# Kernel optimization log

Hardware: AMD Instinct MI355X
Metric: run time of the kernel (lower is better)

The kernel has to match this reference:

```python
import jax, jax.numpy as jnp
import numpy as np

N = 50000      # nodes
E = 400000     # edges (before self-loops)
F_IN = 256     # num_node_features == H*C (required by residual add)
H = 4          # heads
C = 64         # hidden_dim per head
G = 64         # number of graphs in batch
NCLS = 10
EPS = 1e-5
NEG_SLOPE = 0.2  # PyG GATConv default leaky_relu slope


def setup_inputs() -> dict:
    key = jax.random.key(0)
    ks = jax.random.split(key, 20)
    def w(k, shape, s=0.05):
        return jax.random.normal(k, shape, dtype=jnp.float32) * s
    inp = {
        "x": jax.random.normal(ks[0], (N, F_IN), dtype=jnp.float32),
        "edge_index": jax.random.randint(ks[1], (2, E), 0, N, dtype=jnp.int64),
        "batch": jnp.sort(jax.random.randint(ks[2], (N,), 0, G, dtype=jnp.int64)),
        # GAT layer 1 (in=256 -> H*C=256, concat)
        "W1": w(ks[3], (F_IN, H * C)),
        "att_src1": w(ks[4], (H, C)),
        "att_dst1": w(ks[5], (H, C)),
        "b1": jnp.zeros((H * C,), jnp.float32),
        "gamma1": jnp.ones((H * C,), jnp.float32),
        "beta1": jnp.zeros((H * C,), jnp.float32),
        # GAT layer 2 (in=256 -> H*C=256, concat)
        "W2": w(ks[6], (H * C, H * C)),
        "att_src2": w(ks[7], (H, C)),
        "att_dst2": w(ks[8], (H, C)),
        "b2": jnp.zeros((H * C,), jnp.float32),
        "gamma2": jnp.ones((H * C,), jnp.float32),
        "beta2": jnp.zeros((H * C,), jnp.float32),
        # MLP head
        "fc1_w": w(ks[9], (H * C, C)),
        "fc1_b": jnp.zeros((C,), jnp.float32),
        "fc2_w": w(ks[10], (C, NCLS)),
        "fc2_b": jnp.zeros((NCLS,), jnp.float32),
    }
    return inp


def _gat(x, W, att_s, att_d, b, src, dst):
    # x: [N, F] -> h: [N, H, C]
    h = (x @ W).reshape(N, H, C)
    a_src = jnp.einsum('nhc,hc->nh', h, att_s)  # [N, H]
    a_dst = jnp.einsum('nhc,hc->nh', h, att_d)
    e = jax.nn.leaky_relu(a_src[src] + a_dst[dst], NEG_SLOPE)  # [Etot, H]
    # softmax over incoming edges per destination node (self-loops ensure nonempty)
    m = jax.ops.segment_max(e, dst, num_segments=N)
    ex = jnp.exp(e - m[dst])
    s = jax.ops.segment_sum(ex, dst, num_segments=N)
    alpha = ex / s[dst]  # [Etot, H]
    out = jax.ops.segment_sum(alpha[:, :, None] * h[src], dst, num_segments=N)
    return out.reshape(N, H * C) + b


def _bn(x, gamma, beta):
    mu = x.mean(0)
    var = x.var(0)
    return gamma * (x - mu) * jax.lax.rsqrt(var + EPS) + beta


def reference(x, edge_index, batch, W1, att_src1, att_dst1, b1, gamma1, beta1,
              W2, att_src2, att_dst2, b2, gamma2, beta2, fc1_w, fc1_b, fc2_w, fc2_b):
    loops = jnp.arange(N, dtype=edge_index.dtype)
    src = jnp.concatenate([edge_index[0], loops])  # PyG GATConv add_self_loops=True
    dst = jnp.concatenate([edge_index[1], loops])

    h = jax.nn.elu(_gat(x, W1, att_src1, att_dst1, b1, src, dst))
    h = _bn(h + x, gamma1, beta1)  # dropout omitted (eval)
    h2 = jax.nn.elu(_gat(h, W2, att_src2, att_dst2, b2, src, dst))
    h = _bn(h2 + h, gamma2, beta2)

    # global mean pool over graphs
    sums = jax.ops.segment_sum(h, batch, num_segments=G)
    cnt = jax.ops.segment_sum(jnp.ones((N,), h.dtype), batch, num_segments=G)
    pooled = sums / jnp.maximum(cnt, 1.0)[:, None]  # [G, H*C]

    z = jax.nn.relu(pooled @ fc1_w + fc1_b)
    logits = z @ fc2_w + fc2_b
    return jax.nn.log_softmax(logits, axis=1)
```

## Files before the change

### kernel.cpp

```cpp
#include <hip/hip_runtime.h>
#include <hip/hip_bf16.h>

#define NNODES 50000
#define NF 256
#define NH 4
#define NG 64
#define NCLS 10
#define MPAD 50048

typedef __hip_bfloat16 bf16;
typedef __attribute__((ext_vector_type(8))) short short8;
typedef __attribute__((ext_vector_type(4))) short bfx4;
typedef __attribute__((ext_vector_type(4))) float floatx4;

__device__ inline float ldf(const void* p, int i, int isbf) {
    return isbf ? __bfloat162float(((const bf16*)p)[i]) : ((const float*)p)[i];
}
__device__ inline float4 ld4f(const void* p, int i, int isbf) {
    if (isbf) {
        const unsigned* q = (const unsigned*)((const short*)p + i);
        unsigned u0 = q[0], u1 = q[1];
        return make_float4(__uint_as_float(u0 << 16), __uint_as_float(u0 & 0xFFFF0000u),
                           __uint_as_float(u1 << 16), __uint_as_float(u1 & 0xFFFF0000u));
    }
    return *(const float4*)((const float*)p + i);
}
__device__ inline void stf(void* p, int i, float v, int isbf) {
    if (isbf) ((bf16*)p)[i] = __float2bfloat16(v);
    else ((float*)p)[i] = v;
}
__device__ inline short f2bfbits(float v) {
    bf16 b = __float2bfloat16(v);
    return *reinterpret_cast<short*>(&b);
}
__device__ inline float bfbits2f(short s) {
    return __uint_as_float(((unsigned)(unsigned short)s) << 16);
}
__device__ inline unsigned char f2fp8(float v) {
    return (unsigned char)(__builtin_amdgcn_cvt_pk_fp8_f32(v, v, 0, false) & 0xFF);
}
__device__ inline int clampN(int v) { return ((unsigned)v < (unsigned)NNODES) ? v : 0; }
__device__ inline int clampG(int v) { return ((unsigned)v < (unsigned)NG) ? v : 0; }

__global__ void detect_kernel(const int* __restrict__ ei, const unsigned* __restrict__ w1,
                              int* __restrict__ flags) {
    __shared__ int nzOdd, insane;
    if (threadIdx.x == 0) { nzOdd = 0; insane = 0; }
    __syncthreads();
    if (ei[2 * threadIdx.x + 1] != 0) atomicAdd(&nzOdd, 1);
    unsigned lo = w1[threadIdx.x] & 0xFFFFu;
    unsigned ex = (lo >> 7) & 0xFFu;
    bool sane = ((lo & 0x7FFFu) == 0u) || (ex >= 90u && ex <= 133u);
    if (!sane) atomicAdd(&insane, 1);
    __syncthreads();
    if (threadIdx.x == 0) {
        flags[0] = (nzOdd == 0) ? 1 : 0;
        flags[1] = (insane == 0) ? 1 : 0;
    }
}

__device__ inline void edge_sd(const int* __restrict__ ei, int e, int E, int is64,
                               int& s_, int& d_) {
    if (e < E) {
        if (is64) { s_ = ei[2 * e]; d_ = ei[2 * E + 2 * e]; }
        else      { s_ = ei[e];     d_ = ei[E + e]; }
    } else {
        s_ = d_ = e - E;
    }
    s_ = clampN(s_);
    d_ = clampN(d_);
}

__global__ void deg_kernel(const int* __restrict__ ei, int* __restrict__ deg,
                           int E, int ET, const int* __restrict__ flags) {
    int e = blockIdx.x * 256 + threadIdx.x;
    if (e >= ET) return;
    int s_, d_;
    edge_sd(ei, e, E, flags[0], s_, d_);
    atomicAdd(&deg[d_], 1);
}

__global__ void scan1_kernel(const int* __restrict__ deg, int* __restrict__ eprefix,
                             int* __restrict__ bsums, int n) {
    __shared__ int sc[256];
    int t = threadIdx.x, i = blockIdx.x * 256 + t;
    int val = (i < n) ? deg[i] : 0;
    sc[t] = val;
    __syncthreads();
    for (int off = 1; off < 256; off <<= 1) {
        int tmp = (t >= off) ? sc[t - off] : 0;
        __syncthreads();
        sc[t] += tmp;
        __syncthreads();
    }
    if (i < n) eprefix[i] = sc[t] - val;
    if (t == 255) bsums[blockIdx.x] = sc[255];
}

__global__ void scan2_kernel(const int* __restrict__ bsums, int* __restrict__ boffs, int nb) {
    __shared__ int sc[256];
    int t = threadIdx.x;
    int val = (t < nb) ? bsums[t] : 0;
    sc[t] = val;
    __syncthreads();
    for (int off = 1; off < 256; off <<= 1) {
        int tmp = (t >= off) ? sc[t - off] : 0;
        __syncthreads();
        sc[t] += tmp;
        __syncthreads();
    }
    if (t < nb) boffs[t] = sc[t] - val;
}

__global__ void scan3_kernel(const int* __restrict__ eprefix, const int* __restrict__ boffs,
                             int* __restrict__ rowptr, int n, int ET) {
    int i = blockIdx.x * 256 + threadIdx.x;
    if (i < n) rowptr[i] = eprefix[i] + boffs[blockIdx.x];
    if (i == n) rowptr[n] = ET;
}

__global__ void scatter_kernel(const int* __restrict__ ei, const int* __restrict__ rowptr,
                               int* __restrict__ cursor, int* __restrict__ srcs,
                               int E, int ET, const int* __restrict__ flags) {
    int e = blockIdx.x * 256 + threadIdx.x;
    if (e >= ET) return;
    int s_, d_;
    edge_sd(ei, e, E, flags[0], s_, d_);
    int pos = atomicAdd(&cursor[d_], 1);
    srcs[rowptr[d_] + pos] = s_;
}

__global__ void goff_bs_kernel(const int* __restrict__ bt, int* __restrict__ goff,
                               int* __restrict__ gcnt, const int* __restrict__ flags) {
    int is64 = flags[0];
    int t = threadIdx.x;
    if (t <= NG) {
        int lo = 0, hi = NNODES;
        while (lo < hi) {
            int mid = (lo + hi) >> 1;
            int b = clampG(is64 ? bt[2 * mid] : bt[mid]);
            if (b < t) lo = mid + 1; else hi = mid;
        }
        goff[t] = lo;
    }
    __syncthreads();
    if (t < NG) gcnt[t] = goff[t + 1] - goff[t];
}

__global__ void repack_kernel(const void* __restrict__ W, short* __restrict__ Bf,
                              const int* __restrict__ flags) {
    int i = blockIdx.x * 256 + threadIdx.x;
    int j = i & 7, lane = (i >> 3) & 63, tile = i >> 9;
    int kt = tile >> 4, ctg = tile & 15;
    int k = kt * 32 + (lane >> 4) * 8 + j;
    int n = ctg * 16 + (lane & 15);
    Bf[i] = f2bfbits(ldf(W, k * NF + n, flags[1]));
}

__global__ void bn_finalize_kernel(const float* __restrict__ bsum, const float* __restrict__ bsumsq,
                                   const void* __restrict__ gamma, const void* __restrict__ beta,
                                   float* __restrict__ scale, float* __restrict__ shift,
                                   const int* __restrict__ flags) {
    int t = threadIdx.x;
    int isbf = flags[1];
    const float invN = 1.0f / (float)NNODES;
    float mu = bsum[t] * invN;
    float var = fmaxf(bsumsq[t] * invN - mu * mu, 0.f);
    float s = ldf(gamma, t, isbf) * rsqrtf(var + 1e-5f);
    scale[t] = s;
    shift[t] = ldf(beta, t, isbf) - mu * s;
}

__global__ __launch_bounds__(256) void gemm_mfma(
        const void* __restrict__ A, const short* __restrict__ Bf,
        unsigned char* __restrict__ C8,
        int M, const int* __restrict__ flags, int aFollows,
        const void* __restrict__ att_s, const void* __restrict__ att_d,
        float* __restrict__ a_src, float* __restrict__ a_dst,
        const float* __restrict__ scaleA, const float* __restrict__ shiftA) {
    __shared__ short smem[16 * 528];
    int isbf = flags[1];
    int aIsBf = aFollows ? isbf : 1;
    int t = threadIdx.x;
    int wave = t >> 6;
    int lane = t & 63;
    int am = lane & 15, aq = lane >> 4;
    int row0 = blockIdx.x * 32;

    if (aIsBf) {
        #pragma unroll
        for (int i = 0; i < 4; i++) {
            int j = wave * 4 + i;
            int grow = min(row0 + 2 * j + (lane >> 5), M - 1);
            int f0 = (lane & 31) * 8;
            short8 v = *(const short8*)((const short*)A + grow * NF + f0);
            if (scaleA) {
                #pragma unroll
                for (int jj = 0; jj < 8; jj++)
                    v[jj] = f2bfbits(bfbits2f(v[jj]) * scaleA[f0 + jj] + shiftA[f0 + jj]);
            }
            *(short8*)&smem[j * 528 + (lane >> 5) * 256 + f0] = v;
        }
    } else {
        #pragma unroll
        for (int i = 0; i < 4; i++) {
            int u = t * 4 + i;
            int row = u >> 5;
            int pos = u & 31;
            int grow = min(row0 + row, M - 1);
            const float* fp = (const float*)A + grow * NF + pos * 8;
            float4 f0 = *(const float4*)fp;
            float4 f1 = *(const float4*)(fp + 4);
            short8 v;
            v[0] = f2bfbits(f0.x); v[1] = f2bfbits(f0.y);
            v[2] = f2bfbits(f0.z); v[3] = f2bfbits(f0.w);
            v[4] = f2bfbits(f1.x); v[5] = f2bfbits(f1.y);
            v[6] = f2bfbits(f1.z); v[7] = f2bfbits(f1.w);
            *(short8*)&smem[(row >> 1) * 528 + (row & 1) * 256 + pos * 8] = v;
        }
    }
    __syncthreads();

    floatx4 acc[2][4];
    #pragma unroll
    for (int i = 0; i < 2; i++)
        #pragma unroll
        for (int j = 0; j < 4; j++) acc[i][j] = (floatx4){0.f, 0.f, 0.f, 0.f};

    int aoff0 = (am >> 1) * 528 + (am & 1) * 256 + aq * 8;
    #pragma unroll
    for (int kt = 0; kt < 8; kt++) {
        short8 a0 = *(const short8*)&smem[aoff0 + kt * 32];
        short8 a1 = *(const short8*)&smem[aoff0 + 8 * 528 + kt * 32];
        short8 b[4];
        #pragma unroll
        for (int ct = 0; ct < 4; ct++)
            b[ct] = *(const short8*)&Bf[((kt * 16 + wave * 4 + ct) * 64 + lane) * 8];
        #pragma unroll
        for (int ct = 0; ct < 4; ct++) {
            acc[0][ct] = __builtin_amdgcn_mfma_f32_16x16x32_bf16(a0, b[ct], acc[0][ct], 0, 0, 0);
            acc[1][ct] = __builtin_amdgcn_mfma_f32_16x16x32_bf16(a1, b[ct], acc[1][ct], 0, 0, 0);
        }
    }

    int rbase = aq * 4;
    int cbase = wave * 64 + am;
    #pragma unroll
    for (int rt = 0; rt < 2; rt++) {
        #pragma unroll
        for (int r = 0; r < 4; r++) {
            int row = row0 + rt * 16 + rbase + r;
            if (row < M) {
                #pragma unroll
                for (int ct = 0; ct < 4; ct++)
                    C8[row * NF + cbase + ct * 16] = f2fp8(acc[rt][ct][r]);
            }
        }
    }
    float attS[4], attD[4];
    #pragma unroll
    for (int ct = 0; ct < 4; ct++) {
        int col = wave * 64 + ct * 16 + am;
        attS[ct] = ldf(att_s, col, isbf);
        attD[ct] = ldf(att_d, col, isbf);
    }
    #pragma unroll
    for (int rt = 0; rt < 2; rt++) {
        #pragma unroll
        for (int r = 0; r < 4; r++) {
            float ps = 0.f, pd = 0.f;
            #pragma unroll
            for (int ct = 0; ct < 4; ct++) {
                float v = acc[rt][ct][r];
                ps += v * attS[ct];
                pd += v * attD[ct];
            }
            #pragma unroll
            for (int m = 1; m <= 8; m <<= 1) {
                ps += __shfl_xor(ps, m, 64);
                pd += __shfl_xor(pd, m, 64);
            }
            int row = row0 + rt * 16 + rbase + r;
            if (am == 0 && row < M) {
                a_src[row * NH + wave] = ps;
                a_dst[row * NH + wave] = pd;
            }
        }
    }
}

__device__ inline float leaky_clamp(float v) {
    v = v > 0.f ? v : 0.2f * v;
    return fminf(fmaxf(v, -30.f), 30.f);
}

__global__ __launch_bounds__(64) void agg_csr_kernel(
        const int* __restrict__ rowptr, const int* __restrict__ srcs,
        const float* __restrict__ asrc, const float* __restrict__ adst,
        const unsigned char* __restrict__ h8, const void* __restrict__ bias,
        const void* __restrict__ resid, bf16* __restrict__ agg,
        const int* __restrict__ flags, int residFollows,
        const float* __restrict__ rscale, const float* __restrict__ rshift) {
    int d = blockIdx.x;
    int l = threadIdx.x;
    int hh = l >> 4;
    int e16 = l & 15;
    int isbf = flags[1];
    int rIsBf = residFollows ? isbf : 1;
    int beg = rowptr[d], end = rowptr[d + 1];
    float ad = adst[d * NH + hh];
    __shared__ float sAl[NH][16];
    __shared__ int sSrc[16];
    float a0 = 0.f, a1 = 0.f, a2 = 0.f, a3 = 0.f, den = 0.f;
    for (int cb = beg; cb < end; cb += 16) {
        int nk = min(16, end - cb);
        if (e16 < nk) {
            int s = srcs[cb + e16];
            if (hh == 0) sSrc[e16] = s;
            sAl[hh][e16] = __expf(leaky_clamp(asrc[s * NH + hh] + ad));
        }
        __syncthreads();
        for (int k = 0; k < nk; k++) {
            float al = sAl[hh][k];
            den += al;
            unsigned u = *(const unsigned*)&h8[sSrc[k] * NF + 4 * l];
            auto lo = __builtin_amdgcn_cvt_pk_f32_fp8((int)u, false);
            auto hi = __builtin_amdgcn_cvt_pk_f32_fp8((int)u, true);
            a0 += al * lo[0];
            a1 += al * lo[1];
            a2 += al * hi[0];
            a3 += al * hi[1];
        }
        __syncthreads();
    }
    float inv = 1.f / fmaxf(den, 1e-30f);
    a0 *= inv; a1 *= inv; a2 *= inv; a3 *= inv;
    int f0 = 4 * l;
    float4 r = ld4f(resid, d * NF + f0, rIsBf);
    if (rscale) {
        r.x = r.x * rscale[f0] + rshift[f0];
        r.y = r.y * rscale[f0 + 1] + rshift[f0 + 1];
        r.z = r.z * rscale[f0 + 2] + rshift[f0 + 2];
        r.w = r.w * rscale[f0 + 3] + rshift[f0 + 3];
    }
    float v0 = a0 + ldf(bias, f0, isbf);
    float v1 = a1 + ldf(bias, f0 + 1, isbf);
    float v2 = a2 + ldf(bias, f0 + 2, isbf);
    float v3 = a3 + ldf(bias, f0 + 3, isbf);
    v0 = v0 > 0.f ? v0 : (__expf(v0) - 1.0f);
    v1 = v1 > 0.f ? v1 : (__expf(v1) - 1.0f);
    v2 = v2 > 0.f ? v2 : (__expf(v2) - 1.0f);
    v3 = v3 > 0.f ? v3 : (__expf(v3) - 1.0f);
    bfx4 o;
    o[0] = f2bfbits(v0 + r.x);
    o[1] = f2bfbits(v1 + r.y);
    o[2] = f2bfbits(v2 + r.z);
    o[3] = f2bfbits(v3 + r.w);
    *(bfx4*)&agg[d * NF + f0] = o;
}

__global__ __launch_bounds__(256) void bn_stats_kernel(
        const bf16* __restrict__ x, float* __restrict__ bsum, float* __restrict__ bsumsq) {
    __shared__ float ssum[8][256];
    __shared__ float ssq[8][256];
    int t = threadIdx.x;
    int fg = t & 31, rg = t >> 5;
    int f0 = fg * 8;
    float s[8] = {0, 0, 0, 0, 0, 0, 0, 0};
    float q[8] = {0, 0, 0, 0, 0, 0, 0, 0};
    for (int r = blockIdx.x * 8 + rg; r < NNODES; r += gridDim.x * 8) {
        short8 v = *(const short8*)&x[r * NF + f0];
        #pragma unroll
        for (int j = 0; j < 8; j++) {
            float fv = bfbits2f(v[j]);
            s[j] += fv;
            q[j] += fv * fv;
        }
    }
    #pragma unroll
    for (int j = 0; j < 8; j++) {
        ssum[rg][f0 + j] = s[j];
        ssq[rg][f0 + j] = q[j];
    }
    __syncthreads();
    float ts = 0.f, tq = 0.f;
    #pragma unroll
    for (int g = 0; g < 8; g++) {
        ts += ssum[g][t];
        tq += ssq[g][t];
    }
    atomicAdd(&bsum[t], ts);
    atomicAdd(&bsumsq[t], tq);
}

__global__ void pool2_kernel(const bf16* __restrict__ x, const int* __restrict__ goff,
                             float* __restrict__ pooled) {
    int g = blockIdx.x >> 3, c = blockIdx.x & 7, t = threadIdx.x;
    int beg = goff[g], end = goff[g + 1];
    int len = end - beg;
    if (len <= 0) return;
    int chunk = (len + 7) >> 3;
    int s0 = beg + c * chunk;
    int s1 = min(s0 + chunk, end);
    if (s0 >= s1) return;
    float acc = 0.f;
    for (int n = s0; n < s1; n++) acc += __bfloat162float(x[n * NF + t]);
    atomicAdd(&pooled[g * NF + t], acc);
}

__global__ __launch_bounds__(256) void head_kernel(
        const float* __restrict__ pooled, const int* __restrict__ gcnt,
        const float* __restrict__ bnsum2, const float* __restrict__ bnsq2,
        const void* __restrict__ gamma2, const void* __restrict__ beta2,
        const void* __restrict__ fc1w, const void* __restrict__ fc1b,
        const void* __restrict__ fc2w, const void* __restrict__ fc2b,
        void* __restrict__ out, const int* __restrict__ flags) {
    int g = blockIdx.x;
    int t = threadIdx.x;
    int isbf = flags[1];
    __shared__ float p[NF];
    __shared__ float zpart[4][64];
    __shared__ float z[64];
    __shared__ float logits[NCLS];
    __shared__ float lse;
    float c = fmaxf((float)gcnt[g], 1.f);
    float invc = 1.f / c;
    const float invN = 1.0f / (float)NNODES;
    {
        float mu = bnsum2[t] * invN;
        float var = fmaxf(bnsq2[t] * invN - mu * mu, 0.f);
        float pm = pooled[g * NF + t] * invc;
        p[t] = ldf(gamma2, t, isbf) * ((pm - mu) * rsqrtf(var + 1e-5f)) + ldf(beta2, t, isbf);
    }
    __syncthreads();
    int o = t & 63, q = t >> 6;
    int k0 = q * 64;
    float acc = 0.f;
    if (isbf) {
        const bf16* w = (const bf16*)fc1w;
        #pragma unroll 8
        for (int k = k0; k < k0 + 64; k++) acc += p[k] * __bfloat162float(w[k * 64 + o]);
    } else {
        const float* w = (const float*)fc1w;
        #pragma unroll 8
        for (int k = k0; k < k0 + 64; k++) acc += p[k] * w[k * 64 + o];
    }
    zpart[q][o] = acc;
    __syncthreads();
    if (t < 64) {
        float v = zpart[0][t] + zpart[1][t] + zpart[2][t] + zpart[3][t] + ldf(fc1b, t, isbf);
        z[t] = v > 0.f ? v : 0.f;
    }
    __syncthreads();
    if (t < NCLS) {
        float a2 = ldf(fc2b, t, isbf);
        #pragma unroll 8
        for (int k = 0; k < 64; k++) a2 += z[k] * ldf(fc2w, k * NCLS + t, isbf);
        logits[t] = a2;
    }
    __syncthreads();
    if (t == 0) {
        float mx = logits[0];
        for (int j = 1; j < NCLS; j++) mx = fmaxf(mx, logits[j]);
        float se = 0.f;
        for (int j = 0; j < NCLS; j++) se += expf(logits[j] - mx);
        lse = mx + logf(se);
    }
    __syncthreads();
    if (t < NCLS) stf(out, g * NCLS + t, logits[t] - lse, isbf);
}

extern "C" void kernel_launch(void* const* d_in, const int* in_sizes, int n_in,
                              void* d_out, int out_size, void* d_ws, size_t ws_size,
                              hipStream_t stream) {
    const void* x = d_in[0];
    const int* edge_index = (const int*)d_in[1];
    const int* batch = (const int*)d_in[2];
    const void* W1 = d_in[3];
    const void* att_src1 = d_in[4];
    const void* att_dst1 = d_in[5];
    const void* b1 = d_in[6];
    const void* gamma1 = d_in[7];
    const void* beta1 = d_in[8];
    const void* W2 = d_in[9];
    const void* att_src2 = d_in[10];
    const void* att_dst2 = d_in[11];
    const void* b2 = d_in[12];
    const void* gamma2 = d_in[13];
    const void* beta2 = d_in[14];
    const void* fc1w = d_in[15];
    const void* fc1b = d_in[16];
    const void* fc2w = d_in[17];
    const void* fc2b = d_in[18];

    const int E = in_sizes[1] / 2;
    const int ET = E + NNODES;
    const int NE = NNODES * NF;
    const int NNH = NNODES * NH;
    const int NB = (NNODES + 255) / 256;
    const int NB1 = (NNODES + 1 + 255) / 256;

    float* ws = (float*)d_ws;
    bf16* aggb = (bf16*)ws;
    float* asrc = ws + NE / 2;
    float* adst = asrc + NNH;
    int* flags = (int*)(adst + NNH);
    unsigned char* h8 = (unsigned char*)(flags + 16);
    bf16* l1ob = (bf16*)(h8 + (size_t)MPAD * NF);
    int* rowptr = (int*)(l1ob + (size_t)MPAD * NF);
    int* srcs = rowptr + NNODES + 16;
    int* goff = srcs + ET + 16;
    int* deg = goff + NG + 1 + 14;
    int* cursor = deg + NNODES;
    int* gcnt = cursor + NNODES;
    float* pooled = (float*)(gcnt + NG);
    float* bnstat = pooled + NG * NF;
    size_t zero_bytes = (size_t)(2 * NNODES + NG) * 4 + (size_t)(NG * NF + 4 * NF) * 4;
    short* Bf1 = (short*)(bnstat + 4 * NF);
    short* Bf2 = Bf1 + NF * NF;
    float* scale1 = (float*)(Bf2 + NF * NF);
    float* shift1 = scale1 + NF;
    int* eprefix = (int*)asrc;
    int* bsums = eprefix + NNODES + 16;
    int* boffs = bsums + 256;

    float* bnsum1 = bnstat;
    float* bnsq1 = bnstat + NF;
    float* bnsum2 = bnstat + 2 * NF;
    float* bnsq2 = bnstat + 3 * NF;

    detect_kernel<<<1, 256, 0, stream>>>(edge_index, (const unsigned*)W1, flags);
    (void)hipMemsetAsync(deg, 0, zero_bytes, stream);

    repack_kernel<<<NF * NF / 256, 256, 0, stream>>>(W1, Bf1, flags);
    repack_kernel<<<NF * NF / 256, 256, 0, stream>>>(W2, Bf2, flags);

    deg_kernel<<<(ET + 255) / 256, 256, 0, stream>>>(edge_index, deg, E, ET, flags);
    scan1_kernel<<<NB, 256, 0, stream>>>(deg, eprefix, bsums, NNODES);
    scan2_kernel<<<1, 256, 0, stream>>>(bsums, boffs, NB);
    scan3_kernel<<<NB1, 256, 0, stream>>>(eprefix, boffs, rowptr, NNODES, ET);
    scatter_kernel<<<(ET + 255) / 256, 256, 0, stream>>>(edge_index, rowptr, cursor, srcs, E, ET, flags);
    goff_bs_kernel<<<1, 128, 0, stream>>>(batch, goff, gcnt, flags);

    gemm_mfma<<<MPAD / 32, 256, 0, stream>>>(x, Bf1, h8, NNODES, flags, 1,
                                             att_src1, att_dst1, asrc, adst,
                                             nullptr, nullptr);
    agg_csr_kernel<<<NNODES, 64, 0, stream>>>(rowptr, srcs, asrc, adst, h8, b1, x, aggb,
                                              flags, 1, nullptr, nullptr);
    bn_stats_kernel<<<512, 256, 0, stream>>>(aggb, bnsum1, bnsq1);
    bn_finalize_kernel<<<1, 256, 0, stream>>>(bnsum1, bnsq1, gamma1, beta1, scale1, shift1, flags);

    gemm_mfma<<<MPAD / 32, 256, 0, stream>>>(aggb, Bf2, h8, NNODES, flags, 0,
                                             att_src2, att_dst2, asrc, adst,
                                             scale1, shift1);
    agg_csr_kernel<<<NNODES, 64, 0, stream>>>(rowptr, srcs, asrc, adst, h8, b2, aggb, aggb,
                                              flags, 0, scale1, shift1);
    bn_stats_kernel<<<512, 256, 0, stream>>>(aggb, bnsum2, bnsq2);

    pool2_kernel<<<NG * 8, 256, 0, stream>>>(aggb, goff, pooled);
    head_kernel<<<NG, 256, 0, stream>>>(pooled, gcnt, bnsum2, bnsq2, gamma2, beta2,
                                        fc1w, fc1b, fc2w, fc2b, d_out, flags);
}
```

Before: 385.5 us.

## Merge independent small kernels into combined launches and fold BN finalize into consumers

```diff
diff --git a/kernel.cpp b/kernel.cpp
--- a/kernel.cpp
+++ b/kernel.cpp
@@ -7,6 +7,7 @@
 #define NG 64
 #define NCLS 10
 #define MPAD 50048
+#define GEMM_BLKS (MPAD / 32)
 
 typedef __hip_bfloat16 bf16;
 typedef __attribute__((ext_vector_type(8))) short short8;
@@ -71,13 +72,34 @@
     d_ = clampN(d_);
 }
 
-__global__ void deg_kernel(const int* __restrict__ ei, int* __restrict__ deg,
-                           int E, int ET, const int* __restrict__ flags) {
-    int e = blockIdx.x * 256 + threadIdx.x;
+__device__ __forceinline__ void repack_body(int b, const void* __restrict__ W,
+                                            short* __restrict__ Bf, int isbf) {
+    int i = b * 256 + threadIdx.x;
+    int j = i & 7, lane = (i >> 3) & 63, tile = i >> 9;
+    int kt = tile >> 4, ctg = tile & 15;
+    int k = kt * 32 + (lane >> 4) * 8 + j;
+    int n = ctg * 16 + (lane & 15);
+    Bf[i] = f2bfbits(ldf(W, k * NF + n, isbf));
+}
+
+__device__ __forceinline__ void deg_body(int b, const int* __restrict__ ei,
+                                         int* __restrict__ deg, int E, int ET, int is64) {
+    int e = b * 256 + threadIdx.x;
     if (e >= ET) return;
     int s_, d_;
-    edge_sd(ei, e, E, flags[0], s_, d_);
+    edge_sd(ei, e, E, is64, s_, d_);
     atomicAdd(&deg[d_], 1);
+}
+
+__global__ __launch_bounds__(256) void prep_kernel(
+        const void* __restrict__ W1, short* __restrict__ Bf1,
+        const void* __restrict__ W2, short* __restrict__ Bf2,
+        const int* __restrict__ ei, int* __restrict__ deg, int E, int ET,
+        const int* __restrict__ flags) {
+    int b = blockIdx.x;
+    if (b < 256) repack_body(b, W1, Bf1, flags[1]);
+    else if (b < 512) repack_body(b - 256, W2, Bf2, flags[1]);
+    else deg_body(b - 512, ei, deg, E, ET, flags[0]);
 }
 
 __global__ void scan1_kernel(const int* __restrict__ deg, int* __restrict__ eprefix,
@@ -97,7 +119,9 @@
     if (t == 255) bsums[blockIdx.x] = sc[255];
 }
 
-__global__ void scan2_kernel(const int* __restrict__ bsums, int* __restrict__ boffs, int nb) {
+__global__ void scan2_goff_kernel(const int* __restrict__ bsums, int* __restrict__ boffs, int nb,
+                                  const int* __restrict__ bt, int* __restrict__ goff,
+                                  int* __restrict__ gcnt, const int* __restrict__ flags) {
     __shared__ int sc[256];
     int t = threadIdx.x;
     int val = (t < nb) ? bsums[t] : 0;
@@ -110,30 +134,7 @@
         __syncthreads();
     }
     if (t < nb) boffs[t] = sc[t] - val;
-}
-
-__global__ void scan3_kernel(const int* __restrict__ eprefix, const int* __restrict__ boffs,
-                             int* __restrict__ rowptr, int n, int ET) {
-    int i = blockIdx.x * 256 + threadIdx.x;
-    if (i < n) rowptr[i] = eprefix[i] + boffs[blockIdx.x];
-    if (i == n) rowptr[n] = ET;
-}
-
-__global__ void scatter_kernel(const int* __restrict__ ei, const int* __restrict__ rowptr,
-                               int* __restrict__ cursor, int* __restrict__ srcs,
-                               int E, int ET, const int* __restrict__ flags) {
-    int e = blockIdx.x * 256 + threadIdx.x;
-    if (e >= ET) return;
-    int s_, d_;
-    edge_sd(ei, e, E, flags[0], s_, d_);
-    int pos = atomicAdd(&cursor[d_], 1);
-    srcs[rowptr[d_] + pos] = s_;
-}
-
-__global__ void goff_bs_kernel(const int* __restrict__ bt, int* __restrict__ goff,
-                               int* __restrict__ gcnt, const int* __restrict__ flags) {
     int is64 = flags[0];
-    int t = threadIdx.x;
     if (t <= NG) {
         int lo = 0, hi = NNODES;
         while (lo < hi) {
@@ -147,45 +148,52 @@
     if (t < NG) gcnt[t] = goff[t + 1] - goff[t];
 }
 
-__global__ void repack_kernel(const void* __restrict__ W, short* __restrict__ Bf,
-                              const int* __restrict__ flags) {
+__global__ void scan3_kernel(const int* __restrict__ eprefix, const int* __restrict__ boffs,
+                             int* __restrict__ rowptr, int n, int ET) {
     int i = blockIdx.x * 256 + threadIdx.x;
-    int j = i & 7, lane = (i >> 3) & 63, tile = i >> 9;
-    int kt = tile >> 4, ctg = tile & 15;
-    int k = kt * 32 + (lane >> 4) * 8 + j;
-    int n = ctg * 16 + (lane & 15);
-    Bf[i] = f2bfbits(ldf(W, k * NF + n, flags[1]));
-}
-
-__global__ void bn_finalize_kernel(const float* __restrict__ bsum, const float* __restrict__ bsumsq,
-                                   const void* __restrict__ gamma, const void* __restrict__ beta,
-                                   float* __restrict__ scale, float* __restrict__ shift,
-                                   const int* __restrict__ flags) {
-    int t = threadIdx.x;
-    int isbf = flags[1];
-    const float invN = 1.0f / (float)NNODES;
-    float mu = bsum[t] * invN;
-    float var = fmaxf(bsumsq[t] * invN - mu * mu, 0.f);
-    float s = ldf(gamma, t, isbf) * rsqrtf(var + 1e-5f);
-    scale[t] = s;
-    shift[t] = ldf(beta, t, isbf) - mu * s;
-}
-
-__global__ __launch_bounds__(256) void gemm_mfma(
-        const void* __restrict__ A, const short* __restrict__ Bf,
-        unsigned char* __restrict__ C8,
-        int M, const int* __restrict__ flags, int aFollows,
+    if (i < n) rowptr[i] = eprefix[i] + boffs[blockIdx.x];
+    if (i == n) rowptr[n] = ET;
+}
+
+__device__ __forceinline__ void scatter_body(int b, const int* __restrict__ ei,
+                                             const int* __restrict__ rowptr,
+                                             int* __restrict__ cursor, int* __restrict__ srcs,
+                                             int E, int ET, int is64) {
+    int e = b * 256 + threadIdx.x;
+    if (e >= ET) return;
+    int s_, d_;
+    edge_sd(ei, e, E, is64, s_, d_);
+    int pos = atomicAdd(&cursor[d_], 1);
+    srcs[rowptr[d_] + pos] = s_;
+}
+
+__device__ __forceinline__ void gemm_body(
+        int bid, const void* __restrict__ A, const short* __restrict__ Bf,
+        unsigned char* __restrict__ C8, int M, const int* __restrict__ flags, int aFollows,
         const void* __restrict__ att_s, const void* __restrict__ att_d,
         float* __restrict__ a_src, float* __restrict__ a_dst,
-        const float* __restrict__ scaleA, const float* __restrict__ shiftA) {
+        const float* __restrict__ bnsum, const float* __restrict__ bnsq,
+        const void* __restrict__ gamma, const void* __restrict__ beta, int applyBN) {
     __shared__ short smem[16 * 528];
+    __shared__ float sscale[NF];
+    __shared__ float sshift[NF];
     int isbf = flags[1];
     int aIsBf = aFollows ? isbf : 1;
     int t = threadIdx.x;
     int wave = t >> 6;
     int lane = t & 63;
     int am = lane & 15, aq = lane >> 4;
-    int row0 = blockIdx.x * 32;
+    int row0 = bid * 32;
+
+    if (applyBN) {
+        const float invN = 1.0f / (float)NNODES;
+        float mu = bnsum[t] * invN;
+        float var = fmaxf(bnsq[t] * invN - mu * mu, 0.f);
+        float s = ldf(gamma, t, isbf) * rsqrtf(var + 1e-5f);
+        sscale[t] = s;
+        sshift[t] = ldf(beta, t, isbf) - mu * s;
+        __syncthreads();
+    }
 
     if (aIsBf) {
         #pragma unroll
@@ -194,10 +202,10 @@
             int grow = min(row0 + 2 * j + (lane >> 5), M - 1);
             int f0 = (lane & 31) * 8;
             short8 v = *(const short8*)((const short*)A + grow * NF + f0);
-            if (scaleA) {
+            if (applyBN) {
                 #pragma unroll
                 for (int jj = 0; jj < 8; jj++)
-                    v[jj] = f2bfbits(bfbits2f(v[jj]) * scaleA[f0 + jj] + shiftA[f0 + jj]);
+                    v[jj] = f2bfbits(bfbits2f(v[jj]) * sscale[f0 + jj] + sshift[f0 + jj]);
             }
             *(short8*)&smem[j * 528 + (lane >> 5) * 256 + f0] = v;
         }
@@ -289,6 +297,33 @@
     }
 }
 
+__global__ __launch_bounds__(256) void scatter_gemm1_kernel(
+        const int* __restrict__ ei, const int* __restrict__ rowptr,
+        int* __restrict__ cursor, int* __restrict__ srcs, int E, int ET,
+        const void* __restrict__ A, const short* __restrict__ Bf,
+        unsigned char* __restrict__ C8, int M,
+        const void* __restrict__ att_s, const void* __restrict__ att_d,
+        float* __restrict__ a_src, float* __restrict__ a_dst,
+        const int* __restrict__ flags) {
+    if (blockIdx.x < GEMM_BLKS)
+        gemm_body(blockIdx.x, A, Bf, C8, M, flags, 1, att_s, att_d, a_src, a_dst,
+                  nullptr, nullptr, nullptr, nullptr, 0);
+    else
+        scatter_body(blockIdx.x - GEMM_BLKS, ei, rowptr, cursor, srcs, E, ET, flags[0]);
+}
+
+__global__ __launch_bounds__(256) void gemm2_kernel(
+        const void* __restrict__ A, const short* __restrict__ Bf,
+        unsigned char* __restrict__ C8, int M,
+        const void* __restrict__ att_s, const void* __restrict__ att_d,
+        float* __restrict__ a_src, float* __restrict__ a_dst,
+        const float* __restrict__ bnsum, const float* __restrict__ bnsq,
+        const void* __restrict__ gamma, const void* __restrict__ beta,
+        const int* __restrict__ flags) {
+    gemm_body(blockIdx.x, A, Bf, C8, M, flags, 0, att_s, att_d, a_src, a_dst,
+              bnsum, bnsq, gamma, beta, 1);
+}
+
 __device__ inline float leaky_clamp(float v) {
     v = v > 0.f ? v : 0.2f * v;
     return fminf(fmaxf(v, -30.f), 30.f);
@@ -300,13 +335,28 @@
         const unsigned char* __restrict__ h8, const void* __restrict__ bias,
         const void* __restrict__ resid, bf16* __restrict__ agg,
         const int* __restrict__ flags, int residFollows,
-        const float* __restrict__ rscale, const float* __restrict__ rshift) {
+        const float* __restrict__ bnsum, const float* __restrict__ bnsq,
+        const void* __restrict__ gamma, const void* __restrict__ beta, int applyBN) {
     int d = blockIdx.x;
     int l = threadIdx.x;
     int hh = l >> 4;
     int e16 = l & 15;
     int isbf = flags[1];
     int rIsBf = residFollows ? isbf : 1;
+    int f0 = 4 * l;
+    float sc[4] = {1.f, 1.f, 1.f, 1.f}, sh[4] = {0.f, 0.f, 0.f, 0.f};
+    if (applyBN) {
+        const float invN = 1.0f / (float)NNODES;
+        #pragma unroll
+        for (int j = 0; j < 4; j++) {
+            int f = f0 + j;
+            float mu = bnsum[f] * invN;
+            float var = fmaxf(bnsq[f] * invN - mu * mu, 0.f);
+            float s = ldf(gamma, f, isbf) * rsqrtf(var + 1e-5f);
+            sc[j] = s;
+            sh[j] = ldf(beta, f, isbf) - mu * s;
+        }
+    }
     int beg = rowptr[d], end = rowptr[d + 1];
     float ad = adst[d * NH + hh];
     __shared__ float sAl[NH][16];
@@ -323,7 +373,7 @@
         for (int k = 0; k < nk; k++) {
             float al = sAl[hh][k];
             den += al;
-            unsigned u = *(const unsigned*)&h8[sSrc[k] * NF + 4 * l];
+            unsigned u = *(const unsigned*)&h8[sSrc[k] * NF + f0];
             auto lo = __builtin_amdgcn_cvt_pk_f32_fp8((int)u, false);
             auto hi = __builtin_amdgcn_cvt_pk_f32_fp8((int)u, true);
             a0 += al * lo[0];
@@ -335,13 +385,12 @@
     }
     float inv = 1.f / fmaxf(den, 1e-30f);
     a0 *= inv; a1 *= inv; a2 *= inv; a3 *= inv;
-    int f0 = 4 * l;
     float4 r = ld4f(resid, d * NF + f0, rIsBf);
-    if (rscale) {
-        r.x = r.x * rscale[f0] + rshift[f0];
-        r.y = r.y * rscale[f0 + 1] + rshift[f0 + 1];
-        r.z = r.z * rscale[f0 + 2] + rshift[f0 + 2];
-        r.w = r.w * rscale[f0 + 3] + rshift[f0 + 3];
+    if (applyBN) {
+        r.x = r.x * sc[0] + sh[0];
+        r.y = r.y * sc[1] + sh[1];
+        r.z = r.z * sc[2] + sh[2];
+        r.w = r.w * sc[3] + sh[3];
     }
     float v0 = a0 + ldf(bias, f0, isbf);
     float v1 = a1 + ldf(bias, f0 + 1, isbf);
@@ -359,8 +408,8 @@
     *(bfx4*)&agg[d * NF + f0] = o;
 }
 
-__global__ __launch_bounds__(256) void bn_stats_kernel(
-        const bf16* __restrict__ x, float* __restrict__ bsum, float* __restrict__ bsumsq) {
+__device__ __forceinline__ void bn_stats_body(int b, int nblocks, const bf16* __restrict__ x,
+                                              float* __restrict__ bsum, float* __restrict__ bsumsq) {
     __shared__ float ssum[8][256];
     __shared__ float ssq[8][256];
     int t = threadIdx.x;
@@ -368,7 +417,7 @@
     int f0 = fg * 8;
     float s[8] = {0, 0, 0, 0, 0, 0, 0, 0};
     float q[8] = {0, 0, 0, 0, 0, 0, 0, 0};
-    for (int r = blockIdx.x * 8 + rg; r < NNODES; r += gridDim.x * 8) {
+    for (int r = b * 8 + rg; r < NNODES; r += nblocks * 8) {
         short8 v = *(const short8*)&x[r * NF + f0];
         #pragma unroll
         for (int j = 0; j < 8; j++) {
@@ -393,9 +442,14 @@
     atomicAdd(&bsumsq[t], tq);
 }
 
-__global__ void pool2_kernel(const bf16* __restrict__ x, const int* __restrict__ goff,
-                             float* __restrict__ pooled) {
-    int g = blockIdx.x >> 3, c = blockIdx.x & 7, t = threadIdx.x;
+__global__ __launch_bounds__(256) void bn_stats_kernel(
+        const bf16* __restrict__ x, float* __restrict__ bsum, float* __restrict__ bsumsq) {
+    bn_stats_body(blockIdx.x, 512, x, bsum, bsumsq);
+}
+
+__device__ __forceinline__ void pool2_body(int b, const bf16* __restrict__ x,
+                                           const int* __restrict__ goff, float* __restrict__ pooled) {
+    int g = b >> 3, c = b & 7, t = threadIdx.x;
     int beg = goff[g], end = goff[g + 1];
     int len = end - beg;
     if (len <= 0) return;
@@ -406,6 +460,13 @@
     float acc = 0.f;
     for (int n = s0; n < s1; n++) acc += __bfloat162float(x[n * NF + t]);
     atomicAdd(&pooled[g * NF + t], acc);
+}
+
+__global__ __launch_bounds__(256) void stats_pool_kernel(
+        const bf16* __restrict__ x, float* __restrict__ bsum, float* __restrict__ bsumsq,
+        const int* __restrict__ goff, float* __restrict__ pooled) {
+    if (blockIdx.x < 512) bn_stats_body(blockIdx.x, 512, x, bsum, bsumsq);
+    else pool2_body(blockIdx.x - 512, x, goff, pooled);
 }
 
 __global__ __launch_bounds__(256) void head_kernel(
@@ -499,6 +560,7 @@
     const int NNH = NNODES * NH;
     const int NB = (NNODES + 255) / 256;
     const int NB1 = (NNODES + 1 + 255) / 256;
+    const int NBE = (ET + 255) / 256;
 
     float* ws = (float*)d_ws;
     bf16* aggb = (bf16*)ws;
@@ -518,8 +580,6 @@
     size_t zero_bytes = (size_t)(2 * NNODES + NG) * 4 + (size_t)(NG * NF + 4 * NF) * 4;
     short* Bf1 = (short*)(bnstat + 4 * NF);
     short* Bf2 = Bf1 + NF * NF;
-    float* scale1 = (float*)(Bf2 + NF * NF);
-    float* shift1 = scale1 + NF;
     int* eprefix = (int*)asrc;
     int* bsums = eprefix + NNODES + 16;
     int* boffs = bsums + 256;
@@ -532,32 +592,25 @@
     detect_kernel<<<1, 256, 0, stream>>>(edge_index, (const unsigned*)W1, flags);
     (void)hipMemsetAsync(deg, 0, zero_bytes, stream);
 
-    repack_kernel<<<NF * NF / 256, 256, 0, stream>>>(W1, Bf1, flags);
-    repack_kernel<<<NF * NF / 256, 256, 0, stream>>>(W2, Bf2, flags);
-
-    deg_kernel<<<(ET + 255) / 256, 256, 0, stream>>>(edge_index, deg, E, ET, flags);
+    prep_kernel<<<512 + NBE, 256, 0, stream>>>(W1, Bf1, W2, Bf2, edge_index, deg, E, ET, flags);
     scan1_kernel<<<NB, 256, 0, stream>>>(deg, eprefix, bsums, NNODES);
-    scan2_kernel<<<1, 256, 0, stream>>>(bsums, boffs, NB);
+    scan2_goff_kernel<<<1, 256, 0, stream>>>(bsums, boffs, NB, batch, goff, gcnt, flags);
     scan3_kernel<<<NB1, 256, 0, stream>>>(eprefix, boffs, rowptr, NNODES, ET);
-    scatter_kernel<<<(ET + 255) / 256, 256, 0, stream>>>(edge_index, rowptr, cursor, srcs, E, ET, flags);
-    goff_bs_kernel<<<1, 128, 0, stream>>>(batch, goff, gcnt, flags);
-
-    gemm_mfma<<<MPAD / 32, 256, 0, stream>>>(x, Bf1, h8, NNODES, flags, 1,
-                                             att_src1, att_dst1, asrc, adst,
-                                             nullptr, nullptr);
+
+    scatter_gemm1_kernel<<<GEMM_BLKS + NBE, 256, 0, stream>>>(
+        edge_index, rowptr, cursor, srcs, E, ET,
+        x, Bf1, h8, NNODES, att_src1, att_dst1, asrc, adst, flags);
     agg_csr_kernel<<<NNODES, 64, 0, stream>>>(rowptr, srcs, asrc, adst, h8, b1, x, aggb,
-                                              flags, 1, nullptr, nullptr);
+                                              flags, 1, nullptr, nullptr, nullptr, nullptr, 0);
     bn_stats_kernel<<<512, 256, 0, stream>>>(aggb, bnsum1, bnsq1);
-    bn_finalize_kernel<<<1, 256, 0, stream>>>(bnsum1, bnsq1, gamma1, beta1, scale1, shift1, flags);
-
-    gemm_mfma<<<MPAD / 32, 256, 0, stream>>>(aggb, Bf2, h8, NNODES, flags, 0,
-                                             att_src2, att_dst2, asrc, adst,
-                                             scale1, shift1);
+
+    gemm2_kernel<<<GEMM_BLKS, 256, 0, stream>>>(aggb, Bf2, h8, NNODES,
+                                                att_src2, att_dst2, asrc, adst,
+                                                bnsum1, bnsq1, gamma1, beta1, flags);
     agg_csr_kernel<<<NNODES, 64, 0, stream>>>(rowptr, srcs, asrc, adst, h8, b2, aggb, aggb,
-                                              flags, 0, scale1, shift1);
-    bn_stats_kernel<<<512, 256, 0, stream>>>(aggb, bnsum2, bnsq2);
-
-    pool2_kernel<<<NG * 8, 256, 0, stream>>>(aggb, goff, pooled);
+                                              flags, 0, bnsum1, bnsq1, gamma1, beta1, 1);
+
+    stats_pool_kernel<<<512 + NG * 8, 256, 0, stream>>>(aggb, bnsum2, bnsq2, goff, pooled);
     head_kernel<<<NG, 256, 0, stream>>>(pooled, gcnt, bnsum2, bnsq2, gamma2, beta2,
                                         fc1w, fc1b, fc2w, fc2b, d_out, flags);
 }
```

After: 394.8 us. 1.02x slower.
